# Kernel optimization log

Measured on AMD Instinct MI355X. Metric: run time of the kernel, lower is better.

Reference implementation:

```python
import jax, jax.numpy as jnp
import numpy as np

B, S, D, H = 4, 2048, 512, 8
DH = D // H  # depth per head = 64


def setup_inputs() -> dict:
    key = jax.random.key(0)
    ks = jax.random.split(key, 8)
    scale = 1.0 / np.sqrt(D)
    return {
        "query": jax.random.normal(ks[0], (B, S, D), jnp.float32),
        "key": jax.random.normal(ks[1], (B, S, D), jnp.float32),
        "value": jax.random.normal(ks[2], (B, S, D), jnp.float32),
        "mask": jax.random.randint(ks[3], (B, S), 0, 2, jnp.int32),
        "wq_w": jax.random.normal(ks[4], (D, D), jnp.float32) * scale,
        "wq_b": jnp.zeros((D,), jnp.float32),
        "wk_w": jax.random.normal(ks[5], (D, D), jnp.float32) * scale,
        "wk_b": jnp.zeros((D,), jnp.float32),
        "wv_w": jax.random.normal(ks[6], (D, D), jnp.float32) * scale,
        "wv_b": jnp.zeros((D,), jnp.float32),
        "wo_w": jax.random.normal(ks[7], (D, D), jnp.float32) * scale,
        "wo_b": jnp.zeros((D,), jnp.float32),
    }


def _split_heads(x):
    # [B, S, D] -> [B, H, S, DH]
    b, s, _ = x.shape
    return x.reshape(b, s, H, DH).transpose(0, 2, 1, 3)


def reference(query, key, value, mask, wq_w, wq_b, wk_w, wk_b, wv_w, wv_b, wo_w, wo_b):
    q = _split_heads(query @ wq_w + wq_b)   # [B,H,S,DH]
    k = _split_heads(key @ wk_w + wk_b)
    v = _split_heads(value @ wv_w + wv_b)

    scale = 1.0 / jnp.sqrt(jnp.asarray(DH, jnp.float32))
    logits = jnp.einsum('bhqd,bhkd->bhqk', q, k) * scale  # [B,H,S,S]
    # additive key-padding mask: 1 -> masked (adds -1e9)
    m = mask.astype(logits.dtype)[:, None, None, :]  # [B,1,1,S]
    logits = logits + m * -1e9
    weights = jax.nn.softmax(logits, axis=-1)
    attn = jnp.einsum('bhqk,bhkd->bhqd', weights, v)  # [B,H,S,DH]
    attn = attn.transpose(0, 2, 1, 3).reshape(query.shape[0], -1, D)  # [B,S,D]
    return attn @ wo_w + wo_b
```

## Files before the change

### kernel.cpp

```cpp
#include <hip/hip_runtime.h>
#include <stdint.h>

#define QSCALE (0.125f * 1.44269504088896340736f)
#define MASKNEG (-1.442695e9f)

typedef unsigned short u16;
typedef unsigned int u32;
typedef __bf16 bf16x8 __attribute__((ext_vector_type(8)));
typedef float f32x4 __attribute__((ext_vector_type(4)));
typedef u16 u16x8 __attribute__((ext_vector_type(8)));

__device__ __forceinline__ u16 f2bf(float f) {
  u32 u = __float_as_uint(f);
  u += 0x7fffu + ((u >> 16) & 1u);
  return (u16)(u >> 16);
}

__device__ __forceinline__ void gload16(const void* src, void* ldsbase) {
  __builtin_amdgcn_global_load_lds(
      (const __attribute__((address_space(1))) u32*)src,
      (__attribute__((address_space(3))) u32*)ldsbase, 16, 0, 0);
}

__global__ __launch_bounds__(256) void conv_in(const float* __restrict__ q,
                                               const float* __restrict__ k,
                                               const float* __restrict__ v,
                                               u16* __restrict__ dst) {
  const float* src = (blockIdx.z == 0) ? q : (blockIdx.z == 1) ? k : v;
  u16* d = dst + (size_t)blockIdx.z * 4194304;
  size_t i = ((size_t)blockIdx.x * 256 + threadIdx.x) * 8;
  float4 a = *(const float4*)(src + i);
  float4 b = *(const float4*)(src + i + 4);
  u16x8 ov;
  ov[0] = f2bf(a.x); ov[1] = f2bf(a.y); ov[2] = f2bf(a.z); ov[3] = f2bf(a.w);
  ov[4] = f2bf(b.x); ov[5] = f2bf(b.y); ov[6] = f2bf(b.z); ov[7] = f2bf(b.w);
  *(u16x8*)(d + i) = ov;
}

__global__ __launch_bounds__(256) void conv_w(const float* __restrict__ wq,
                                              const float* __restrict__ wk,
                                              const float* __restrict__ wv,
                                              const float* __restrict__ wo,
                                              u16* __restrict__ wT) {
  const float* src = (blockIdx.z == 0) ? wq : (blockIdx.z == 1) ? wk
                    : (blockIdx.z == 2) ? wv : wo;
  u16* dst = wT + (size_t)blockIdx.z * 262144;
  __shared__ float t[64][65];
  const int n0 = blockIdx.x * 64, k0 = blockIdx.y * 64;
  const int lr = threadIdx.x >> 6, lc = threadIdx.x & 63;
#pragma unroll
  for (int it = 0; it < 16; ++it) {
    const int row = it * 4 + lr;
    t[row][lc] = src[(size_t)(k0 + row) * 512 + n0 + lc];
  }
  __syncthreads();
#pragma unroll
  for (int it = 0; it < 16; ++it) {
    const int row = it * 4 + lr;
    dst[(size_t)(n0 + row) * 512 + k0 + lc] = f2bf(t[lc][row]);
  }
}

__device__ __forceinline__ void gemm_core(const u16* __restrict__ A,
                                          const u16* __restrict__ Bt,
                                          int m0, int n0, char* lds,
                                          f32x4 acc[4][4]) {
  const int tid = threadIdx.x;
  const int lane = tid & 63;
  const int wave = tid >> 6;
  const int wm = wave >> 1, wn = wave & 1;
  const int srow = tid >> 3;
  const int sc16 = tid & 7;

  auto stage = [&](int buf, int kt) {
    const int k0 = kt * 64;
    char* base = lds + buf * 32768;
#pragma unroll
    for (int c = 0; c < 4; ++c) {
      const int row = c * 32 + srow;
      const int xc = (sc16 ^ (row & 7)) << 3;
      gload16(A + (size_t)(m0 + row) * 512 + k0 + xc,
              base + c * 4096 + (wave << 10));
      gload16(Bt + (size_t)(n0 + row) * 512 + k0 + xc,
              base + 16384 + c * 4096 + (wave << 10));
    }
  };

  auto compute = [&](int buf) {
    const char* bA = lds + buf * 32768;
    const char* bB = bA + 16384;
#pragma unroll
    for (int kk = 0; kk < 2; ++kk) {
      const int c16 = kk * 4 + (lane >> 4);
      bf16x8 av[4], bv[4];
#pragma unroll
      for (int i = 0; i < 4; ++i) {
        const int row = wm * 64 + i * 16 + (lane & 15);
        av[i] = *(const bf16x8*)(bA + row * 128 + ((c16 ^ (row & 7)) << 4));
      }
#pragma unroll
      for (int j = 0; j < 4; ++j) {
        const int row = wn * 64 + j * 16 + (lane & 15);
        bv[j] = *(const bf16x8*)(bB + row * 128 + ((c16 ^ (row & 7)) << 4));
      }
#pragma unroll
      for (int i = 0; i < 4; ++i)
#pragma unroll
        for (int j = 0; j < 4; ++j)
          acc[i][j] = __builtin_amdgcn_mfma_f32_16x16x32_bf16(av[i], bv[j],
                                                              acc[i][j], 0, 0, 0);
    }
  };

  stage(0, 0);
  __syncthreads();
#pragma unroll
  for (int kt = 0; kt < 8; ++kt) {
    const int cur = kt & 1;
    if (kt < 7) stage(cur ^ 1, kt + 1);
    compute(cur);
    __syncthreads();
  }
}

__global__ __launch_bounds__(256) void gemm_qkv(
    const u16* __restrict__ xq, const u16* __restrict__ xk,
    const u16* __restrict__ xv, const u16* __restrict__ wT,
    const float* __restrict__ bq, const float* __restrict__ bk,
    const float* __restrict__ bv, u16* __restrict__ qws, u16* __restrict__ kws,
    u16* __restrict__ vTw) {
  __shared__ __align__(16) char lds[65536];
  const int z = blockIdx.z;
  const u16* A = (z == 0) ? xq : (z == 1) ? xk : xv;
  const u16* Bt = wT + (size_t)z * 262144;
  const float* bias = (z == 0) ? bq : (z == 1) ? bk : bv;
  const int m0 = blockIdx.y * 128, n0 = blockIdx.x * 128;
  f32x4 acc[4][4] = {};
  gemm_core(A, Bt, m0, n0, lds, acc);
  const int lane = threadIdx.x & 63, wave = threadIdx.x >> 6;
  const int wm = wave >> 1, wn = wave & 1;
#pragma unroll
  for (int j = 0; j < 4; ++j) {
    const int n = n0 + wn * 64 + j * 16 + (lane & 15);
    const float bn = bias[n];
    const int h = n >> 6, dh = n & 63;
#pragma unroll
    for (int i = 0; i < 4; ++i) {
#pragma unroll
      for (int r = 0; r < 4; ++r) {
        const int rg = m0 + wm * 64 + i * 16 + ((lane >> 4) << 2) + r;
        const int b = rg >> 11, s = rg & 2047;
        const int bh = b * 8 + h;
        const float val = acc[i][j][r] + bn;
        if (z == 0) {
          qws[((size_t)bh * 2048 + s) * 64 + dh] = f2bf(val * QSCALE);
        } else if (z == 1) {
          kws[((size_t)bh * 2048 + s) * 64 + dh] = f2bf(val);
        } else {
          vTw[((size_t)bh * 64 + dh) * 2048 + s] = f2bf(val);
        }
      }
    }
  }
}

__global__ __launch_bounds__(256) void attn_fwd(const u16* __restrict__ qws,
                                                const u16* __restrict__ kws,
                                                const u16* __restrict__ vTw,
                                                const int* __restrict__ mask,
                                                u16* __restrict__ attn) {
  __shared__ __align__(16) char ldsK[16384];
  __shared__ __align__(16) char ldsV[16384];
  __shared__ __align__(16) char plds[16384];
  __shared__ float mbias[2][64];
  const int qt = blockIdx.x;
  const int bh = blockIdx.y;
  const int b = bh >> 3;
  const int tid = threadIdx.x;
  const int lane = tid & 63, wave = tid >> 6;
  const int srow = tid >> 3, sc16 = tid & 7;

  const u16* qbase = qws + ((size_t)bh * 2048 + qt * 128 + wave * 32) * 64;
  bf16x8 qa[2][2];
#pragma unroll
  for (int rg = 0; rg < 2; ++rg)
#pragma unroll
    for (int kk = 0; kk < 2; ++kk)
      qa[rg][kk] = *(const bf16x8*)(qbase + (rg * 16 + (lane & 15)) * 64 +
                                    kk * 32 + (lane >> 4) * 8);

  auto stage = [&](int buf, int kt) {
#pragma unroll
    for (int c = 0; c < 2; ++c) {
      const int row = c * 32 + srow;
      const int xc = (sc16 ^ (row & 7)) << 3;
      gload16(kws + ((size_t)bh * 2048 + kt * 64 + row) * 64 + xc,
              ldsK + buf * 8192 + c * 4096 + (wave << 10));
      gload16(vTw + ((size_t)bh * 64 + row) * 2048 + kt * 64 + xc,
              ldsV + buf * 8192 + c * 4096 + (wave << 10));
    }
    if (tid < 64)
      mbias[buf][tid] = mask[b * 2048 + kt * 64 + tid] ? MASKNEG : 0.0f;
  };

  float rs[2][4] = {};
  f32x4 o[2][4] = {};
  char* pw = plds + wave * 4096;

  stage(0, 0);
  __syncthreads();

  for (int kt = 0; kt < 32; ++kt) {
    const int cur = kt & 1;
    if (kt < 31) stage(cur ^ 1, kt + 1);

    const char* kb = ldsK + cur * 8192;
    f32x4 sv[2][4] = {};
    __builtin_amdgcn_s_setprio(1);
#pragma unroll
    for (int t = 0; t < 4; ++t) {
      const int row = t * 16 + (lane & 15);
#pragma unroll
      for (int kk = 0; kk < 2; ++kk) {
        const int c16 = kk * 4 + (lane >> 4);
        const bf16x8 kf =
            *(const bf16x8*)(kb + row * 128 + ((c16 ^ (row & 7)) << 4));
        sv[0][t] = __builtin_amdgcn_mfma_f32_16x16x32_bf16(qa[0][kk], kf, sv[0][t], 0, 0, 0);
        sv[1][t] = __builtin_amdgcn_mfma_f32_16x16x32_bf16(qa[1][kk], kf, sv[1][t], 0, 0, 0);
      }
    }
    __builtin_amdgcn_s_setprio(0);

#pragma unroll
    for (int t = 0; t < 4; ++t) {
      const float mb = mbias[cur][t * 16 + (lane & 15)];
#pragma unroll
      for (int rg = 0; rg < 2; ++rg)
#pragma unroll
        for (int r = 0; r < 4; ++r) {
          const float p = __builtin_amdgcn_exp2f(sv[rg][t][r] + mb);
          rs[rg][r] += p;
          const int prow = rg * 16 + ((lane >> 4) << 2) + r;
          const int off =
              prow * 128 + (((t * 32 + (lane & 15) * 2)) ^ ((prow & 7) << 4));
          *(__bf16*)(pw + off) = (__bf16)p;
        }
    }

    const char* vb = ldsV + cur * 8192;
    __builtin_amdgcn_s_setprio(1);
#pragma unroll
    for (int kk = 0; kk < 2; ++kk) {
      const int c16 = kk * 4 + (lane >> 4);
      bf16x8 pa[2];
#pragma unroll
      for (int rg = 0; rg < 2; ++rg) {
        const int prow = rg * 16 + (lane & 15);
        pa[rg] = *(const bf16x8*)(pw + prow * 128 +
                                  ((kk * 64 + (lane >> 4) * 16) ^ ((prow & 7) << 4)));
      }
#pragma unroll
      for (int dt = 0; dt < 4; ++dt) {
        const int vrow = dt * 16 + (lane & 15);
        const bf16x8 vf =
            *(const bf16x8*)(vb + vrow * 128 + ((c16 ^ (vrow & 7)) << 4));
        o[0][dt] = __builtin_amdgcn_mfma_f32_16x16x32_bf16(pa[0], vf, o[0][dt], 0, 0, 0);
        o[1][dt] = __builtin_amdgcn_mfma_f32_16x16x32_bf16(pa[1], vf, o[1][dt], 0, 0, 0);
      }
    }
    __builtin_amdgcn_s_setprio(0);
    __syncthreads();
  }

  float invl[2][4];
#pragma unroll
  for (int rg = 0; rg < 2; ++rg)
#pragma unroll
    for (int r = 0; r < 4; ++r) {
      float s = rs[rg][r];
      s += __shfl_xor(s, 1);
      s += __shfl_xor(s, 2);
      s += __shfl_xor(s, 4);
      s += __shfl_xor(s, 8);
      invl[rg][r] = 1.0f / s;
    }
  const int h = bh & 7;
#pragma unroll
  for (int rg = 0; rg < 2; ++rg) {
    const int sq0 = qt * 128 + wave * 32 + rg * 16 + ((lane >> 4) << 2);
#pragma unroll
    for (int dt = 0; dt < 4; ++dt) {
      const int dcol = h * 64 + dt * 16 + (lane & 15);
#pragma unroll
      for (int r = 0; r < 4; ++r)
        attn[(size_t)(b * 2048 + sq0 + r) * 512 + dcol] =
            f2bf(o[rg][dt][r] * invl[rg][r]);
    }
  }
}

__global__ __launch_bounds__(256) void gemm_out(const u16* __restrict__ attn,
                                                const u16* __restrict__ woT,
                                                const float* __restrict__ bo,
                                                float* __restrict__ out) {
  __shared__ __align__(16) char lds[65536];
  const int m0 = blockIdx.y * 128, n0 = blockIdx.x * 128;
  f32x4 acc[4][4] = {};
  gemm_core(attn, woT, m0, n0, lds, acc);
  const int lane = threadIdx.x & 63, wave = threadIdx.x >> 6;
  const int wm = wave >> 1, wn = wave & 1;
#pragma unroll
  for (int j = 0; j < 4; ++j) {
    const int n = n0 + wn * 64 + j * 16 + (lane & 15);
    const float bn = bo[n];
#pragma unroll
    for (int i = 0; i < 4; ++i) {
      const int rbase = m0 + wm * 64 + i * 16 + ((lane >> 4) << 2);
#pragma unroll
      for (int r = 0; r < 4; ++r)
        out[(size_t)(rbase + r) * 512 + n] = acc[i][j][r] + bn;
    }
  }
}

extern "C" void kernel_launch(void* const* d_in, const int* in_sizes, int n_in,
                              void* d_out, int out_size, void* d_ws,
                              size_t ws_size, hipStream_t stream) {
  (void)in_sizes; (void)n_in; (void)out_size; (void)ws_size;
  const float* q = (const float*)d_in[0];
  const float* k = (const float*)d_in[1];
  const float* v = (const float*)d_in[2];
  const int* mask = (const int*)d_in[3];
  const float* wq = (const float*)d_in[4];
  const float* bq = (const float*)d_in[5];
  const float* wk = (const float*)d_in[6];
  const float* bk = (const float*)d_in[7];
  const float* wv = (const float*)d_in[8];
  const float* bv = (const float*)d_in[9];
  const float* wo = (const float*)d_in[10];
  const float* bo = (const float*)d_in[11];

  u16* xq = (u16*)d_ws;
  u16* xk = xq + 4194304;
  u16* xv = xk + 4194304;
  u16* wT = xv + 4194304;
  u16* qws = wT + 1048576;
  u16* kws = qws + 4194304;
  u16* vTw = kws + 4194304;
  u16* attn = xq;
  float* out = (float*)d_out;

  conv_in<<<dim3(2048, 1, 3), 256, 0, stream>>>(q, k, v, xq);
  conv_w<<<dim3(8, 8, 4), 256, 0, stream>>>(wq, wk, wv, wo, wT);
  gemm_qkv<<<dim3(4, 64, 3), 256, 0, stream>>>(xq, xk, xv, wT, bq, bk, bv, qws,
                                               kws, vTw);
  attn_fwd<<<dim3(16, 32), 256, 0, stream>>>(qws, kws, vTw, mask, attn);
  gemm_out<<<dim3(4, 64), 256, 0, stream>>>(attn, wT + 786432, bo, out);
}
```

Measured before the change: 121.6 us.

## Split attention keys across two wave groups with LDS reduction of partial outputs

The attention kernel now uses 512 threads per block covering 64 query rows. Two halves of 4 waves each process half of the key sequence independently, and their partial outputs and row sums are combined through LDS at the end. The grid doubles to 1024 blocks, which raises parallelism and occupancy across the CUs. Mask bias is now read straight from global memory per tile instead of being staged in LDS. The cost is that each block loads K/V for only 64 queries, halving reuse per K/V load, plus an extra LDS reduction step.

```diff
diff --git a/kernel.cpp b/kernel.cpp
--- a/kernel.cpp
+++ b/kernel.cpp
@@ -164,58 +164,63 @@
   }
 }
 
-__global__ __launch_bounds__(256) void attn_fwd(const u16* __restrict__ qws,
+__global__ __launch_bounds__(512) void attn_fwd(const u16* __restrict__ qws,
                                                 const u16* __restrict__ kws,
                                                 const u16* __restrict__ vTw,
                                                 const int* __restrict__ mask,
                                                 u16* __restrict__ attn) {
-  __shared__ __align__(16) char ldsK[16384];
-  __shared__ __align__(16) char ldsV[16384];
+  __shared__ __align__(16) char ldsK[32768];
+  __shared__ __align__(16) char ldsV[32768];
   __shared__ __align__(16) char plds[16384];
-  __shared__ float mbias[2][64];
   const int qt = blockIdx.x;
   const int bh = blockIdx.y;
   const int b = bh >> 3;
   const int tid = threadIdx.x;
   const int lane = tid & 63, wave = tid >> 6;
-  const int srow = tid >> 3, sc16 = tid & 7;
-
-  const u16* qbase = qws + ((size_t)bh * 2048 + qt * 128 + wave * 32) * 64;
-  bf16x8 qa[2][2];
-#pragma unroll
-  for (int rg = 0; rg < 2; ++rg)
-#pragma unroll
-    for (int kk = 0; kk < 2; ++kk)
-      qa[rg][kk] = *(const bf16x8*)(qbase + (rg * 16 + (lane & 15)) * 64 +
-                                    kk * 32 + (lane >> 4) * 8);
-
-  auto stage = [&](int buf, int kt) {
+  const int half = wave >> 2, wl = wave & 3;
+
+  const u16* qbase = qws + ((size_t)bh * 2048 + qt * 64 + wl * 16) * 64;
+  bf16x8 qa[2];
+#pragma unroll
+  for (int kk = 0; kk < 2; ++kk)
+    qa[kk] = *(const bf16x8*)(qbase + (lane & 15) * 64 + kk * 32 + (lane >> 4) * 8);
+
+  char* myK = ldsK + half * 16384;
+  char* myV = ldsV + half * 16384;
+  const int srow = wl * 8 + (lane >> 3);
+  const int sc16 = lane & 7;
+
+  auto stage = [&](int buf, int ktg) {
 #pragma unroll
     for (int c = 0; c < 2; ++c) {
       const int row = c * 32 + srow;
       const int xc = (sc16 ^ (row & 7)) << 3;
-      gload16(kws + ((size_t)bh * 2048 + kt * 64 + row) * 64 + xc,
-              ldsK + buf * 8192 + c * 4096 + (wave << 10));
-      gload16(vTw + ((size_t)bh * 64 + row) * 2048 + kt * 64 + xc,
-              ldsV + buf * 8192 + c * 4096 + (wave << 10));
-    }
-    if (tid < 64)
-      mbias[buf][tid] = mask[b * 2048 + kt * 64 + tid] ? MASKNEG : 0.0f;
+      gload16(kws + ((size_t)bh * 2048 + ktg * 64 + row) * 64 + xc,
+              myK + buf * 8192 + c * 4096 + (wl << 10));
+      gload16(vTw + ((size_t)bh * 64 + row) * 2048 + ktg * 64 + xc,
+              myV + buf * 8192 + c * 4096 + (wl << 10));
+    }
   };
 
-  float rs[2][4] = {};
-  f32x4 o[2][4] = {};
-  char* pw = plds + wave * 4096;
-
-  stage(0, 0);
+  float rs[4] = {};
+  f32x4 o[4] = {};
+  char* pw = plds + wave * 2048;
+
+  stage(0, half * 16);
   __syncthreads();
 
-  for (int kt = 0; kt < 32; ++kt) {
+  for (int kt = 0; kt < 16; ++kt) {
     const int cur = kt & 1;
-    if (kt < 31) stage(cur ^ 1, kt + 1);
-
-    const char* kb = ldsK + cur * 8192;
-    f32x4 sv[2][4] = {};
+    const int ktg = half * 16 + kt;
+    float mb[4];
+#pragma unroll
+    for (int t = 0; t < 4; ++t)
+      mb[t] = mask[b * 2048 + ktg * 64 + t * 16 + (lane & 15)] ? MASKNEG : 0.0f;
+
+    if (kt < 15) stage(cur ^ 1, ktg + 1);
+
+    const char* kb = myK + cur * 8192;
+    f32x4 sv[4] = {};
     __builtin_amdgcn_s_setprio(1);
 #pragma unroll
     for (int t = 0; t < 4; ++t) {
@@ -225,76 +230,89 @@
         const int c16 = kk * 4 + (lane >> 4);
         const bf16x8 kf =
             *(const bf16x8*)(kb + row * 128 + ((c16 ^ (row & 7)) << 4));
-        sv[0][t] = __builtin_amdgcn_mfma_f32_16x16x32_bf16(qa[0][kk], kf, sv[0][t], 0, 0, 0);
-        sv[1][t] = __builtin_amdgcn_mfma_f32_16x16x32_bf16(qa[1][kk], kf, sv[1][t], 0, 0, 0);
+        sv[t] = __builtin_amdgcn_mfma_f32_16x16x32_bf16(qa[kk], kf, sv[t], 0, 0, 0);
       }
     }
     __builtin_amdgcn_s_setprio(0);
 
 #pragma unroll
     for (int t = 0; t < 4; ++t) {
-      const float mb = mbias[cur][t * 16 + (lane & 15)];
-#pragma unroll
-      for (int rg = 0; rg < 2; ++rg)
-#pragma unroll
-        for (int r = 0; r < 4; ++r) {
-          const float p = __builtin_amdgcn_exp2f(sv[rg][t][r] + mb);
-          rs[rg][r] += p;
-          const int prow = rg * 16 + ((lane >> 4) << 2) + r;
-          const int off =
-              prow * 128 + (((t * 32 + (lane & 15) * 2)) ^ ((prow & 7) << 4));
-          *(__bf16*)(pw + off) = (__bf16)p;
-        }
-    }
-
-    const char* vb = ldsV + cur * 8192;
+#pragma unroll
+      for (int r = 0; r < 4; ++r) {
+        const float p = __builtin_amdgcn_exp2f(sv[t][r] + mb[t]);
+        rs[r] += p;
+        const int prow = ((lane >> 4) << 2) + r;
+        const int off =
+            prow * 128 + (((t * 32 + (lane & 15) * 2)) ^ ((prow & 7) << 4));
+        *(__bf16*)(pw + off) = (__bf16)p;
+      }
+    }
+
+    const char* vb = myV + cur * 8192;
     __builtin_amdgcn_s_setprio(1);
 #pragma unroll
     for (int kk = 0; kk < 2; ++kk) {
-      const int c16 = kk * 4 + (lane >> 4);
-      bf16x8 pa[2];
-#pragma unroll
-      for (int rg = 0; rg < 2; ++rg) {
-        const int prow = rg * 16 + (lane & 15);
-        pa[rg] = *(const bf16x8*)(pw + prow * 128 +
-                                  ((kk * 64 + (lane >> 4) * 16) ^ ((prow & 7) << 4)));
-      }
+      const int arow = lane & 15;
+      const bf16x8 pa = *(const bf16x8*)(pw + arow * 128 +
+                            ((kk * 64 + (lane >> 4) * 16) ^ ((arow & 7) << 4)));
 #pragma unroll
       for (int dt = 0; dt < 4; ++dt) {
         const int vrow = dt * 16 + (lane & 15);
+        const int c16 = kk * 4 + (lane >> 4);
         const bf16x8 vf =
             *(const bf16x8*)(vb + vrow * 128 + ((c16 ^ (vrow & 7)) << 4));
-        o[0][dt] = __builtin_amdgcn_mfma_f32_16x16x32_bf16(pa[0], vf, o[0][dt], 0, 0, 0);
-        o[1][dt] = __builtin_amdgcn_mfma_f32_16x16x32_bf16(pa[1], vf, o[1][dt], 0, 0, 0);
+        o[dt] = __builtin_amdgcn_mfma_f32_16x16x32_bf16(pa, vf, o[dt], 0, 0, 0);
       }
     }
     __builtin_amdgcn_s_setprio(0);
     __syncthreads();
   }
 
-  float invl[2][4];
-#pragma unroll
-  for (int rg = 0; rg < 2; ++rg)
-#pragma unroll
-    for (int r = 0; r < 4; ++r) {
-      float s = rs[rg][r];
-      s += __shfl_xor(s, 1);
-      s += __shfl_xor(s, 2);
-      s += __shfl_xor(s, 4);
-      s += __shfl_xor(s, 8);
-      invl[rg][r] = 1.0f / s;
-    }
-  const int h = bh & 7;
-#pragma unroll
-  for (int rg = 0; rg < 2; ++rg) {
-    const int sq0 = qt * 128 + wave * 32 + rg * 16 + ((lane >> 4) << 2);
+  float lsum[4];
+#pragma unroll
+  for (int r = 0; r < 4; ++r) {
+    float s = rs[r];
+    s += __shfl_xor(s, 1);
+    s += __shfl_xor(s, 2);
+    s += __shfl_xor(s, 4);
+    s += __shfl_xor(s, 8);
+    lsum[r] = s;
+  }
+
+  float* oSh = (float*)ldsK;
+  float* lSh = (float*)ldsV;
+  if (half == 1) {
+#pragma unroll
+    for (int dt = 0; dt < 4; ++dt)
+#pragma unroll
+      for (int r = 0; r < 4; ++r)
+        oSh[wl * 1024 + (((lane >> 4) << 2) + r) * 64 + dt * 16 + (lane & 15)] =
+            o[dt][r];
+    if ((lane & 15) == 0) {
+#pragma unroll
+      for (int r = 0; r < 4; ++r)
+        lSh[wl * 16 + ((lane >> 4) << 2) + r] = lsum[r];
+    }
+  }
+  __syncthreads();
+  if (half == 0) {
+    const int h = bh & 7;
+    float invl[4];
+#pragma unroll
+    for (int r = 0; r < 4; ++r)
+      invl[r] = 1.0f / (lsum[r] + lSh[wl * 16 + ((lane >> 4) << 2) + r]);
+    const int sq0 = qt * 64 + wl * 16 + ((lane >> 4) << 2);
 #pragma unroll
     for (int dt = 0; dt < 4; ++dt) {
       const int dcol = h * 64 + dt * 16 + (lane & 15);
 #pragma unroll
-      for (int r = 0; r < 4; ++r)
-        attn[(size_t)(b * 2048 + sq0 + r) * 512 + dcol] =
-            f2bf(o[rg][dt][r] * invl[rg][r]);
+      for (int r = 0; r < 4; ++r) {
+        const float val =
+            (o[dt][r] +
+             oSh[wl * 1024 + (((lane >> 4) << 2) + r) * 64 + dt * 16 + (lane & 15)]) *
+            invl[r];
+        attn[(size_t)(b * 2048 + sq0 + r) * 512 + dcol] = f2bf(val);
+      }
     }
   }
 }
@@ -354,6 +372,6 @@
   conv_w<<<dim3(8, 8, 4), 256, 0, stream>>>(wq, wk, wv, wo, wT);
   gemm_qkv<<<dim3(4, 64, 3), 256, 0, stream>>>(xq, xk, xv, wT, bq, bk, bv, qws,
                                                kws, vTw);
-  attn_fwd<<<dim3(16, 32), 256, 0, stream>>>(qws, kws, vTw, mask, attn);
+  attn_fwd<<<dim3(32, 32), 512, 0, stream>>>(qws, kws, vTw, mask, attn);
   gemm_out<<<dim3(4, 64), 256, 0, stream>>>(attn, wT + 786432, bo, out);
 }
```

Result: no change. 120.4 us (-0.9%).
